# Kernel optimization log

Hardware: AMD Instinct MI355X
Metric: run time of the kernel (lower is better)

The kernel has to match this reference:

```python
import jax, jax.numpy as jnp
import numpy as np

IN_H, IN_W = 256, 256
CHANNELS = 128
KH, KW = 3, 3
PAD = 1
OUT_H = IN_H + 2 * PAD - KH + 1  # 256
OUT_W = IN_W + 2 * PAD - KW + 1  # 256
L = OUT_H * OUT_W


def setup_inputs() -> dict:
    key = jax.random.key(0)
    k1, k2 = jax.random.split(key)
    input_tensor = jax.random.normal(k1, (1, CHANNELS, IN_H, IN_W), dtype=jnp.float32)
    # Parameter(out_h*out_w, kh*kw); init scale ~ 1/sqrt(C*kh*kw) as in reset_parameters
    stddev = 1.0 / np.sqrt(CHANNELS * KH * KW)
    weights = jax.random.uniform(k2, (L, KH * KW), dtype=jnp.float32,
                                 minval=-stddev, maxval=stddev)
    return {"input_tensor": input_tensor, "weights": weights}


def _unfold(x):
    # torch.nn.Unfold(kernel=(KH,KW), padding=PAD, stride=1):
    # output (1, C*KH*KW, L) with feature dim ordered (C, kh, kw) slowest->fastest.
    xp = jnp.pad(x, ((0, 0), (0, 0), (PAD, PAD), (PAD, PAD)))
    # small fixed loop over 9 kernel offsets (not a data-dim loop)
    patches = jnp.stack(
        [xp[:, :, i:i + OUT_H, j:j + OUT_W] for i in range(KH) for j in range(KW)],
        axis=2,
    )  # (1, C, KH*KW, OUT_H, OUT_W)
    return patches.reshape(1, CHANNELS * KH * KW, L)


def reference(input_tensor, weights):
    unfolded = _unfold(input_tensor)                       # (1, C*kk, L)
    # Faithful to the original: permute then raw row-major reshape to (1, C, L, kk)
    unfolded = jnp.transpose(unfolded, (0, 2, 1)).reshape(1, CHANNELS, L, KH * KW)
    out = jnp.sum(unfolded * weights, axis=-1)             # (1, C, L)
    out = out.reshape(1, CHANNELS, OUT_H, OUT_W)
    return out[:, :, :IN_H, :IN_W]
```

## Files before the change

### kernel.cpp

```cpp
#include <hip/hip_runtime.h>


#define NCH  128
#define C_CH 32
#define W_CH 8
#define COLS 10
#define CPAD 11
#define RSTR (C_CH*CPAD)
#define RING 16
#define NIT  32
#define DIST 12
#define LAND 8
#define NSTG 21

__global__ __launch_bounds__(256)
void conv2d_local_kernel(const float* __restrict__ in,
                         const float* __restrict__ wgt,
                         float* __restrict__ out) {
    __shared__ float li[RING * RSTR];

    const int bid = blockIdx.x;
    const int swz = (bid & 7) * 128 + (bid >> 3);
    const int cs  = swz >> 8;
    const int ws  = (swz & 255) >> 3;
    const int hs  = swz & 7;

    const int c0 = cs * C_CH;
    const int w0 = ws * W_CH;
    const int h0 = hs * NIT;

    const int t  = threadIdx.x;
    const int c  = t & 31;
    const int wo = t >> 5;

    const float* wb = wgt + (size_t)((w0 + wo) * NCH + c0 + c) * 9;
    float wp0[9], wp1[9];
    #pragma unroll
    for (int k = 0; k < 9; ++k) {
        wp0[k] = wb[k];
        wp1[k] = wb[(size_t)256 * NCH * 9 + k];
    }

    const int cs0 = t / 10,          col0 = t - cs0 * 10;
    const int cs1 = (256 + t) / 10,  col1 = (256 + t) - cs1 * 10;
    const bool has1 = t < 64;
    const int gw0 = w0 - 1 + col0;  const bool okw0 = (unsigned)gw0 < 256u;
    const int gw1 = w0 - 1 + col1;  const bool okw1 = (unsigned)gw1 < 256u;
    const float* in0 = in + (((size_t)(c0 + cs0)) << 16) + (okw0 ? gw0 : 0);
    const float* in1 = in + (((size_t)(c0 + cs1)) << 16) + (okw1 ? gw1 : 0);
    const int ld0 = cs0 * CPAD + col0;
    const int ld1 = cs1 * CPAD + col1;

    for (int e = t; e < 13 * C_CH * COLS; e += 256) {
        int r   = e / (C_CH * COLS);
        int re  = e - r * (C_CH * COLS);
        int cc  = re / COLS;
        int col = re - cc * COLS;
        int gh  = h0 - 1 + r;
        int gw  = w0 - 1 + col;
        float v = 0.f;
        if ((unsigned)gh < 256u && (unsigned)gw < 256u)
            v = in[(((size_t)(c0 + cc)) << 16) + (gh << 8) + gw];
        li[((gh + RING) & 15) * RSTR + cc * CPAD + col] = v;
    }
    __syncthreads();

    const float* lrd = li + c * CPAD + wo;
    float A0, A1, A2, B0, B1, B2;
    { const float* p = lrd + 15 * RSTR; A0 = p[0]; A1 = p[1]; A2 = p[2]; }
    { const float* p = lrd;             B0 = p[0]; B1 = p[1]; B2 = p[2]; }

    float sv0[NIT], sv1[NIT];
    const size_t obase = (size_t)((h0 << 8) + w0 + wo) * NCH + c0 + c;

    #pragma unroll
    for (int i = 0; i < NIT; ++i) {
        if (i < NSTG) {
            const int gh = h0 + DIST + i;
            float v0 = 0.f, v1 = 0.f;
            if (okw0 && (unsigned)gh < 256u) v0 = in0[gh << 8];
            if (has1 && okw1 && (unsigned)gh < 256u) v1 = in1[gh << 8];
            sv0[i] = v0; sv1[i] = v1;
        }
        float C0, C1, C2;
        { const float* p = lrd + ((i + 1) & 15) * RSTR; C0 = p[0]; C1 = p[1]; C2 = p[2]; }
        const float* wp = (i & 1) ? wp1 : wp0;
        float acc = fmaf(wp[0], A0, fmaf(wp[1], A1, fmaf(wp[2], A2,
                    fmaf(wp[3], B0, fmaf(wp[4], B1, fmaf(wp[5], B2,
                    fmaf(wp[6], C0, fmaf(wp[7], C1, wp[8] * C2))))))));
        out[obase + (size_t)i * (256 * NCH)] = acc;
        A0 = B0; A1 = B1; A2 = B2;
        B0 = C0; B1 = C1; B2 = C2;
        if (i >= LAND && i - LAND < NSTG) {
            const int j = i - LAND;
            li[((DIST + j) & 15) * RSTR + ld0] = sv0[j];
            if (has1) li[((DIST + j) & 15) * RSTR + ld1] = sv1[j];
        }
        __syncthreads();
    }
}

extern "C" void kernel_launch(void* const* d_in, const int* in_sizes, int n_in,
                              void* d_out, int out_size, void* d_ws, size_t ws_size,
                              hipStream_t stream) {
    (void)in_sizes; (void)n_in; (void)d_ws; (void)ws_size; (void)out_size;
    const float* in = (const float*)d_in[0];
    const float* w  = (const float*)d_in[1];
    float* out      = (float*)d_out;
    conv2d_local_kernel<<<dim3(1024), dim3(256), 0, stream>>>(in, w, out);
}
```

Measured before the change: 102.6 us.

## Halve rows per block, process two output rows per barrier with register prefetch

Each block now covers 16 output rows instead of 32 and the grid doubles to 2048 blocks. The LDS ring shrinks to 8 rows. The main loop computes two output rows per iteration, so there is one barrier per two rows. The deep 21-row register staging is replaced by a two-row register prefetch that is issued one iteration ahead. The aims are more parallelism, fewer syncs and lower register pressure. In exchange the halo overhead per block rises and the prefetch distance is shorter, which exposes more load latency.

```diff
diff --git a/kernel.cpp b/kernel.cpp
--- a/kernel.cpp
+++ b/kernel.cpp
@@ -3,15 +3,11 @@
 
 #define NCH  128
 #define C_CH 32
-#define W_CH 8
 #define COLS 10
 #define CPAD 11
 #define RSTR (C_CH*CPAD)
-#define RING 16
-#define NIT  32
-#define DIST 12
-#define LAND 8
-#define NSTG 21
+#define RING 8
+#define NIT  16
 
 __global__ __launch_bounds__(256)
 void conv2d_local_kernel(const float* __restrict__ in,
@@ -20,13 +16,13 @@
     __shared__ float li[RING * RSTR];
 
     const int bid = blockIdx.x;
-    const int swz = (bid & 7) * 128 + (bid >> 3);
-    const int cs  = swz >> 8;
-    const int ws  = (swz & 255) >> 3;
-    const int hs  = swz & 7;
+    const int swz = (bid & 7) * 256 + (bid >> 3);
+    const int cs  = swz >> 9;
+    const int ws  = (swz >> 4) & 31;
+    const int hs  = swz & 15;
 
     const int c0 = cs * C_CH;
-    const int w0 = ws * W_CH;
+    const int w0 = ws * 8;
     const int h0 = hs * NIT;
 
     const int t  = threadIdx.x;
@@ -36,13 +32,10 @@
     const float* wb = wgt + (size_t)((w0 + wo) * NCH + c0 + c) * 9;
     float wp0[9], wp1[9];
     #pragma unroll
-    for (int k = 0; k < 9; ++k) {
-        wp0[k] = wb[k];
-        wp1[k] = wb[(size_t)256 * NCH * 9 + k];
-    }
+    for (int k = 0; k < 9; ++k) { wp0[k] = wb[k]; wp1[k] = wb[256 * NCH * 9 + k]; }
 
-    const int cs0 = t / 10,          col0 = t - cs0 * 10;
-    const int cs1 = (256 + t) / 10,  col1 = (256 + t) - cs1 * 10;
+    const int cs0 = t / COLS,         col0 = t - cs0 * COLS;
+    const int cs1 = (256 + t) / COLS, col1 = (256 + t) - cs1 * COLS;
     const bool has1 = t < 64;
     const int gw0 = w0 - 1 + col0;  const bool okw0 = (unsigned)gw0 < 256u;
     const int gw1 = w0 - 1 + col1;  const bool okw1 = (unsigned)gw1 < 256u;
@@ -51,7 +44,7 @@
     const int ld0 = cs0 * CPAD + col0;
     const int ld1 = cs1 * CPAD + col1;
 
-    for (int e = t; e < 13 * C_CH * COLS; e += 256) {
+    for (int e = t; e < 7 * C_CH * COLS; e += 256) {
         int r   = e / (C_CH * COLS);
         int re  = e - r * (C_CH * COLS);
         int cc  = re / COLS;
@@ -61,41 +54,63 @@
         float v = 0.f;
         if ((unsigned)gh < 256u && (unsigned)gw < 256u)
             v = in[(((size_t)(c0 + cc)) << 16) + (gh << 8) + gw];
-        li[((gh + RING) & 15) * RSTR + cc * CPAD + col] = v;
+        li[(gh & 7) * RSTR + cc * CPAD + col] = v;
     }
     __syncthreads();
 
     const float* lrd = li + c * CPAD + wo;
     float A0, A1, A2, B0, B1, B2;
-    { const float* p = lrd + 15 * RSTR; A0 = p[0]; A1 = p[1]; A2 = p[2]; }
-    { const float* p = lrd;             B0 = p[0]; B1 = p[1]; B2 = p[2]; }
+    { const float* p = lrd + 7 * RSTR; A0 = p[0]; A1 = p[1]; A2 = p[2]; }
+    { const float* p = lrd;            B0 = p[0]; B1 = p[1]; B2 = p[2]; }
+    __syncthreads();
 
-    float sv0[NIT], sv1[NIT];
-    const size_t obase = (size_t)((h0 << 8) + w0 + wo) * NCH + c0 + c;
+    float ra0, ra1, rb0, rb1;
+    {
+        const int g6 = (h0 + 6) << 8, g7 = (h0 + 7) << 8;
+        ra0 = okw0 ? in0[g6] : 0.f;
+        ra1 = (has1 && okw1) ? in1[g6] : 0.f;
+        rb0 = okw0 ? in0[g7] : 0.f;
+        rb1 = (has1 && okw1) ? in1[g7] : 0.f;
+    }
 
     #pragma unroll
-    for (int i = 0; i < NIT; ++i) {
-        if (i < NSTG) {
-            const int gh = h0 + DIST + i;
-            float v0 = 0.f, v1 = 0.f;
-            if (okw0 && (unsigned)gh < 256u) v0 = in0[gh << 8];
-            if (has1 && okw1 && (unsigned)gh < 256u) v1 = in1[gh << 8];
-            sv0[i] = v0; sv1[i] = v1;
+    for (int i = 0; i < NIT / 2; ++i) {
+        const int r6 = 2 * i + 6, r7 = 2 * i + 7;
+
+        float C0, C1, C2, D0, D1, D2;
+        { const float* p = lrd + ((2 * i + 1) & 7) * RSTR; C0 = p[0]; C1 = p[1]; C2 = p[2]; }
+        { const float* p = lrd + ((2 * i + 2) & 7) * RSTR; D0 = p[0]; D1 = p[1]; D2 = p[2]; }
+
+        li[(r6 & 7) * RSTR + ld0] = ra0;
+        li[(r7 & 7) * RSTR + ld0] = rb0;
+        if (has1) {
+            li[(r6 & 7) * RSTR + ld1] = ra1;
+            li[(r7 & 7) * RSTR + ld1] = rb1;
         }
-        float C0, C1, C2;
-        { const float* p = lrd + ((i + 1) & 15) * RSTR; C0 = p[0]; C1 = p[1]; C2 = p[2]; }
-        const float* wp = (i & 1) ? wp1 : wp0;
-        float acc = fmaf(wp[0], A0, fmaf(wp[1], A1, fmaf(wp[2], A2,
-                    fmaf(wp[3], B0, fmaf(wp[4], B1, fmaf(wp[5], B2,
-                    fmaf(wp[6], C0, fmaf(wp[7], C1, wp[8] * C2))))))));
-        out[obase + (size_t)i * (256 * NCH)] = acc;
-        A0 = B0; A1 = B1; A2 = B2;
-        B0 = C0; B1 = C1; B2 = C2;
-        if (i >= LAND && i - LAND < NSTG) {
-            const int j = i - LAND;
-            li[((DIST + j) & 15) * RSTR + ld0] = sv0[j];
-            if (has1) li[((DIST + j) & 15) * RSTR + ld1] = sv1[j];
+
+        {
+            int gh = h0 + r6 + 2;
+            bool okh = gh < 256;
+            ra0 = (okw0 && okh) ? in0[gh << 8] : 0.f;
+            ra1 = (has1 && okw1 && okh) ? in1[gh << 8] : 0.f;
+            gh = h0 + r7 + 2;
+            okh = gh < 256;
+            rb0 = (okw0 && okh) ? in0[gh << 8] : 0.f;
+            rb1 = (has1 && okw1 && okh) ? in1[gh << 8] : 0.f;
         }
+
+        float acc0 = fmaf(wp0[0], A0, fmaf(wp0[1], A1, fmaf(wp0[2], A2,
+                     fmaf(wp0[3], B0, fmaf(wp0[4], B1, fmaf(wp0[5], B2,
+                     fmaf(wp0[6], C0, fmaf(wp0[7], C1, wp0[8] * C2))))))));
+        float acc1 = fmaf(wp1[0], B0, fmaf(wp1[1], B1, fmaf(wp1[2], B2,
+                     fmaf(wp1[3], C0, fmaf(wp1[4], C1, fmaf(wp1[5], C2,
+                     fmaf(wp1[6], D0, fmaf(wp1[7], D1, wp1[8] * D2))))))));
+        const int h = h0 + 2 * i;
+        out[(size_t)(((h)     << 8) + w0 + wo) * NCH + c0 + c] = acc0;
+        out[(size_t)(((h + 1) << 8) + w0 + wo) * NCH + c0 + c] = acc1;
+
+        A0 = C0; A1 = C1; A2 = C2;
+        B0 = D0; B1 = D1; B2 = D2;
         __syncthreads();
     }
 }
@@ -107,5 +122,5 @@
     const float* in = (const float*)d_in[0];
     const float* w  = (const float*)d_in[1];
     float* out      = (float*)d_out;
-    conv2d_local_kernel<<<dim3(1024), dim3(256), 0, stream>>>(in, w, out);
+    conv2d_local_kernel<<<dim3(2048), dim3(256), 0, stream>>>(in, w, out);
 }
```

After: 101.3 us. About the same (-1.3%).
